# Kernel tuning notes

Hardware: AMD Instinct MI355X
Metric: run time of the kernel (lower is better)

Reference implementation:

```python
import jax, jax.numpy as jnp
import numpy as np

N, D, Z, T, K = 100000, 128, 128, 1024, 256
HID = 512
D_IN = D + 2 * Z  # concat of ctx, z_ctx_pe, z_tgt_pe


def setup_inputs() -> dict:
    key = jax.random.key(0)
    ks = jax.random.split(key, 12)
    inp = {
        'pe': jax.random.normal(ks[0], (N, 4), jnp.float32),
        'context_embedding': jax.random.normal(ks[1], (N, D), jnp.float32),
        'target_embedding': jax.random.normal(ks[2], (N, D), jnp.float32),
        # padded 2-hop subgraph node ids per target (precomputed k_hop_subgraph)
        'sub_nodes': jax.random.randint(ks[3], (T, K), 0, N, jnp.int32),
        'sub_counts': jax.random.randint(ks[4], (T,), 1, K + 1, jnp.int32),
        'target_nodes': jax.random.randint(ks[5], (T,), 0, N, jnp.int32),
        # params
        'z': jax.random.normal(ks[6], (1, Z), jnp.float32) * 0.1,
        'W_pe': jax.random.normal(ks[7], (4, Z), jnp.float32) * 0.5,
        'W1': jax.random.normal(ks[8], (D_IN, HID), jnp.float32) * (1.0 / np.sqrt(D_IN)),
        'b1': jnp.zeros((HID,), jnp.float32),
        'W2': jax.random.normal(ks[9], (HID, D), jnp.float32) * (1.0 / np.sqrt(HID)),
        'b2': jnp.zeros((D,), jnp.float32),
    }
    return inp


def reference(pe, context_embedding, target_embedding, sub_nodes, sub_counts,
              target_nodes, z, W_pe, W1, b1, W2, b2):
    # position_encoding = pe_projector(laplacian_eigenvector_pe)  [N, Z]
    pos_enc = pe @ W_pe
    # gather per-subgraph quantities (batched over T targets, padded to K)
    sub_ctx = context_embedding[sub_nodes]            # [T, K, D]
    z_ctx_pe = z + pos_enc[sub_nodes]                 # [T, K, Z]
    z_tgt_pe = z + pos_enc[target_nodes][:, None, :]  # [T, 1, Z] -> broadcast
    z_tgt_pe = jnp.broadcast_to(z_tgt_pe, z_ctx_pe.shape)
    agg = jnp.concatenate([sub_ctx, z_ctx_pe, z_tgt_pe], axis=-1)  # [T, K, D_IN]
    # predictor MLP
    pred = jax.nn.relu(agg @ W1 + b1) @ W2 + b2       # [T, K, D]
    tgt = target_embedding[target_nodes][:, None, :]  # [T, 1, D]
    sq = (pred - tgt) ** 2                            # [T, K, D]
    counts = jnp.maximum(sub_counts, 1)
    mask = (jnp.arange(K)[None, :] < counts[:, None]).astype(sq.dtype)  # [T, K]
    # per-target MSELoss (mean over n_sub * D elements), summed over targets
    per_target = jnp.sum(sq * mask[:, :, None], axis=(1, 2)) / (counts.astype(sq.dtype) * D)
    return jnp.sum(per_target)
```

## Files before the change

kernel.cpp:

```cpp
#include <hip/hip_runtime.h>
#include <hip/hip_bf16.h>

#define NN   100000
#define DD   128
#define ZZ   128
#define TT   1024
#define KK   256
#define HIDD 512

typedef __attribute__((ext_vector_type(8))) short  short8;
typedef __attribute__((ext_vector_type(4))) float  f32x4;

__device__ inline unsigned short f2bf(float f) {
    union { float f; unsigned int u; } x; x.f = f;
    unsigned int r = x.u + 0x7fffu + ((x.u >> 16) & 1u);
    return (unsigned short)(r >> 16);
}
__device__ inline void load_lds16(const void* g, void* l) {
    __builtin_amdgcn_global_load_lds((const __attribute__((address_space(1))) unsigned int*)g,
                                     (__attribute__((address_space(3))) unsigned int*)l, 16, 0, 0);
}

__global__ __launch_bounds__(256) void prep_tables(
    const float* __restrict__ pe, const float* __restrict__ ctx,
    const float* __restrict__ z, const float* __restrict__ wpe,
    unsigned short* __restrict__ ctx_bf, unsigned short* __restrict__ zpe_bf) {
    int g = blockIdx.x * 256 + threadIdx.x;
    if (g >= NN * 16) return;
    int n = g >> 4, j8 = (g & 15) << 3;
    float p0 = pe[n * 4 + 0], p1 = pe[n * 4 + 1], p2 = pe[n * 4 + 2], p3 = pe[n * 4 + 3];
    float4 c0 = *(const float4*)(ctx + (size_t)n * 128 + j8);
    float4 c1 = *(const float4*)(ctx + (size_t)n * 128 + j8 + 4);
    float4 z0 = *(const float4*)(z + j8);
    float4 z1 = *(const float4*)(z + j8 + 4);
    float4 wa0 = *(const float4*)(wpe + 0 * ZZ + j8), wa1 = *(const float4*)(wpe + 0 * ZZ + j8 + 4);
    float4 wb0 = *(const float4*)(wpe + 1 * ZZ + j8), wb1 = *(const float4*)(wpe + 1 * ZZ + j8 + 4);
    float4 wc0 = *(const float4*)(wpe + 2 * ZZ + j8), wc1 = *(const float4*)(wpe + 2 * ZZ + j8 + 4);
    float4 wd0 = *(const float4*)(wpe + 3 * ZZ + j8), wd1 = *(const float4*)(wpe + 3 * ZZ + j8 + 4);
    float zp[8], cv[8];
    zp[0] = z0.x + p0 * wa0.x + p1 * wb0.x + p2 * wc0.x + p3 * wd0.x;
    zp[1] = z0.y + p0 * wa0.y + p1 * wb0.y + p2 * wc0.y + p3 * wd0.y;
    zp[2] = z0.z + p0 * wa0.z + p1 * wb0.z + p2 * wc0.z + p3 * wd0.z;
    zp[3] = z0.w + p0 * wa0.w + p1 * wb0.w + p2 * wc0.w + p3 * wd0.w;
    zp[4] = z1.x + p0 * wa1.x + p1 * wb1.x + p2 * wc1.x + p3 * wd1.x;
    zp[5] = z1.y + p0 * wa1.y + p1 * wb1.y + p2 * wc1.y + p3 * wd1.y;
    zp[6] = z1.z + p0 * wa1.z + p1 * wb1.z + p2 * wc1.z + p3 * wd1.z;
    zp[7] = z1.w + p0 * wa1.w + p1 * wb1.w + p2 * wc1.w + p3 * wd1.w;
    cv[0] = c0.x; cv[1] = c0.y; cv[2] = c0.z; cv[3] = c0.w;
    cv[4] = c1.x; cv[5] = c1.y; cv[6] = c1.z; cv[7] = c1.w;
    short8 sz, sc;
#pragma unroll
    for (int i = 0; i < 8; ++i) { sz[i] = (short)f2bf(zp[i]); sc[i] = (short)f2bf(cv[i]); }
    *(short8*)(zpe_bf + (size_t)g * 8) = sz;
    *(short8*)(ctx_bf + (size_t)g * 8) = sc;
}

__global__ __launch_bounds__(256) void pack_ct(
    const float* __restrict__ W1, const float* __restrict__ W2,
    const float* __restrict__ pe, const float* __restrict__ z, const float* __restrict__ wpe,
    const int* __restrict__ target_nodes, const float* __restrict__ b1,
    unsigned short* __restrict__ w1p, unsigned short* __restrict__ w2p, float* __restrict__ ct_g) {
    __shared__ float zp[8][128];
    int tid = threadIdx.x;
    if (blockIdx.x < 768) {
        int g = blockIdx.x * 256 + tid;
        if (g < 256 * HIDD) {
            int e = g & 7, l = (g >> 3) & 63, tile = g >> 9;
            int ntg = tile & 7, rem = tile >> 3;
            int kc = rem & 7, hc = rem >> 3;
            int k = kc * 32 + (l >> 4) * 8 + e;
            int n = hc * 128 + ntg * 16 + (l & 15);
            w1p[g] = f2bf(W1[(size_t)k * HIDD + n]);
        } else {
            int q = g - 256 * HIDD;
            int e = q & 7, l = (q >> 3) & 63, tile = q >> 9;
            int ntg = tile & 7, kcg = tile >> 3;
            int k = kcg * 32 + (l >> 4) * 8 + e;
            int n = ntg * 16 + (l & 15);
            w2p[q] = f2bf(W2[(size_t)k * DD + n]);
        }
        return;
    }
    int b = blockIdx.x - 768;
#pragma unroll
    for (int q = 0; q < 4; ++q) {
        int idx = q * 256 + tid;
        int t8 = idx >> 7, zz = idx & 127;
        int tgt = target_nodes[b * 8 + t8];
        zp[t8][zz] = z[zz] + pe[tgt * 4 + 0] * wpe[zz] + pe[tgt * 4 + 1] * wpe[128 + zz]
                           + pe[tgt * 4 + 2] * wpe[256 + zz] + pe[tgt * 4 + 3] * wpe[384 + zz];
    }
    __syncthreads();
    int j0 = tid, j1 = tid + 256;
    float a0[8], a1[8];
    float bb0 = b1[j0], bb1 = b1[j1];
#pragma unroll
    for (int t8 = 0; t8 < 8; ++t8) { a0[t8] = bb0; a1[t8] = bb1; }
#pragma unroll 8
    for (int zz = 0; zz < 128; ++zz) {
        float w0 = W1[(size_t)(256 + zz) * HIDD + j0];
        float w1 = W1[(size_t)(256 + zz) * HIDD + j1];
#pragma unroll
        for (int t8 = 0; t8 < 8; ++t8) { a0[t8] += zp[t8][zz] * w0; a1[t8] += zp[t8][zz] * w1; }
    }
#pragma unroll
    for (int t8 = 0; t8 < 8; ++t8) {
        ct_g[(size_t)(b * 8 + t8) * HIDD + j0] = a0[t8];
        ct_g[(size_t)(b * 8 + t8) * HIDD + j1] = a1[t8];
    }
}

__global__ __launch_bounds__(256) void mp_jepa_main(
    const unsigned short* __restrict__ ctx_bf,
    const unsigned short* __restrict__ zpe_bf,
    const unsigned short* __restrict__ w1p,
    const unsigned short* __restrict__ w2p,
    const float* __restrict__ ct_g,
    const float* __restrict__ target_embedding,
    const int* __restrict__ sub_nodes,
    const int* __restrict__ sub_counts,
    const int* __restrict__ target_nodes,
    const float* __restrict__ b2,
    float* __restrict__ out) {
    const int bid = blockIdx.x;
    const int t = bid >> 2, kt = bid & 3;
    const int k0 = kt * 64;
    int cnt = sub_counts[t]; if (cnt < 1) cnt = 1;
    if (k0 >= cnt) return;
    const int tgt = target_nodes[t];

    __shared__ __align__(16) unsigned short ctxT[64 * 128];
    __shared__ __align__(16) unsigned short zpeT[64 * 128];
    __shared__ __align__(16) unsigned short hT[64 * 128];
    __shared__ float cts[HIDD];
    __shared__ float tgte[DD];
    __shared__ float b2s[DD];
    __shared__ float red[4];

    const int tid = threadIdx.x;
    const int w = tid >> 6, l = tid & 63;
    const int lo = l & 15, hi = l >> 4;

    {
        const char* cc = (const char*)ctx_bf;
        const char* zc = (const char*)zpe_bf;
        const int base = t * KK + k0;
#pragma unroll
        for (int it = 0; it < 4; ++it) {
            int rgrp = it * 16 + (w << 2);
            int row  = rgrp + hi;
            int node = sub_nodes[base + row];
            int soff = (lo << 4) ^ ((row & 7) << 4);
            load_lds16(cc + (size_t)node * 256 + soff, (char*)ctxT + rgrp * 256);
            load_lds16(zc + (size_t)node * 256 + soff, (char*)zpeT + rgrp * 256);
        }
    }
    if (tid < 128) {
        tgte[tid] = target_embedding[(size_t)tgt * 128 + tid];
        b2s[tid]  = b2[tid];
    }
    cts[tid]       = ct_g[(size_t)t * HIDD + tid];
    cts[tid + 256] = ct_g[(size_t)t * HIDD + tid + 256];
    __syncthreads();

    const short8* w1v = (const short8*)w1p;
    const short8* w2v = (const short8*)w2p;

    f32x4 accP[4][2];
#pragma unroll
    for (int rg = 0; rg < 4; ++rg)
#pragma unroll
        for (int nt = 0; nt < 2; ++nt) accP[rg][nt] = (f32x4){0.f, 0.f, 0.f, 0.f};

    for (int hc = 0; hc < 4; ++hc) {
        short8 wA[16];
#pragma unroll
        for (int i = 0; i < 16; ++i) {
            int kc = i >> 1, nt = i & 1;
            wA[i] = w1v[((((hc << 3) + kc) << 3) + (w << 1) + nt) * 64 + l];
        }
        f32x4 acc1[4][2];
#pragma unroll
        for (int nt = 0; nt < 2; ++nt) {
            f32x4 cv = *(const f32x4*)&cts[(hc << 7) + (((w << 1) + nt) << 4) + (hi << 2)];
#pragma unroll
            for (int rg = 0; rg < 4; ++rg) acc1[rg][nt] = cv;
        }
#pragma unroll
        for (int kc = 0; kc < 8; ++kc) {
            const unsigned short* src = (kc < 4) ? ctxT : zpeT;
            int cb = ((kc & 3) << 6) + (hi << 4);
            short8 a[4];
#pragma unroll
            for (int rg = 0; rg < 4; ++rg) {
                int row = (rg << 4) + lo;
                a[rg] = *(const short8*)(src + ((row * 256 + (cb ^ ((row & 7) << 4))) >> 1));
            }
#pragma unroll
            for (int rg = 0; rg < 4; ++rg) {
                acc1[rg][0] = __builtin_amdgcn_mfma_f32_16x16x32_bf16(wA[(kc << 1) + 0], a[rg], acc1[rg][0], 0, 0, 0);
                acc1[rg][1] = __builtin_amdgcn_mfma_f32_16x16x32_bf16(wA[(kc << 1) + 1], a[rg], acc1[rg][1], 0, 0, 0);
            }
        }

        short8 wB[8];
#pragma unroll
        for (int i = 0; i < 8; ++i) {
            int kc2 = i >> 1, nt = i & 1;
            wB[i] = w2v[((((hc << 2) + kc2) << 3) + (w << 1) + nt) * 64 + l];
        }

        __syncthreads();
#pragma unroll
        for (int nt = 0; nt < 2; ++nt) {
            int cbase = (((w << 1) + nt) << 5) + (hi << 3);
#pragma unroll
            for (int rg = 0; rg < 4; ++rg) {
                int row = (rg << 4) + lo;
                f32x4 v = acc1[rg][nt];
                float v0 = v[0] > 0.f ? v[0] : 0.f;
                float v1 = v[1] > 0.f ? v[1] : 0.f;
                float v2 = v[2] > 0.f ? v[2] : 0.f;
                float v3 = v[3] > 0.f ? v[3] : 0.f;
                uint2 p;
                p.x = (unsigned int)f2bf(v0) | ((unsigned int)f2bf(v1) << 16);
                p.y = (unsigned int)f2bf(v2) | ((unsigned int)f2bf(v3) << 16);
                *(uint2*)((char*)hT + row * 256 + (cbase ^ ((row & 7) << 4))) = p;
            }
        }
        __syncthreads();

#pragma unroll
        for (int kc2 = 0; kc2 < 4; ++kc2) {
            int cb = (kc2 << 6) + (hi << 4);
#pragma unroll
            for (int rg = 0; rg < 4; ++rg) {
                int row = (rg << 4) + lo;
                short8 a = *(const short8*)(hT + ((row * 256 + (cb ^ ((row & 7) << 4))) >> 1));
                accP[rg][0] = __builtin_amdgcn_mfma_f32_16x16x32_bf16(a, wB[(kc2 << 1) + 0], accP[rg][0], 0, 0, 0);
                accP[rg][1] = __builtin_amdgcn_mfma_f32_16x16x32_bf16(a, wB[(kc2 << 1) + 1], accP[rg][1], 0, 0, 0);
            }
        }
    }

    float s = 0.f;
#pragma unroll
    for (int nt = 0; nt < 2; ++nt) {
        int col = (w << 5) + (nt << 4) + lo;
        float bb = b2s[col] - tgte[col];
#pragma unroll
        for (int rg = 0; rg < 4; ++rg) {
#pragma unroll
            for (int r = 0; r < 4; ++r) {
                int row = (rg << 4) + (hi << 2) + r;
                float d = accP[rg][nt][r] + bb;
                if (k0 + row < cnt) s += d * d;
            }
        }
    }
#pragma unroll
    for (int off = 32; off > 0; off >>= 1) s += __shfl_xor(s, off, 64);
    if (l == 0) red[w] = s;
    __syncthreads();
    if (tid == 0) {
        float tot = (red[0] + red[1] + red[2] + red[3]) / ((float)cnt * 128.0f);
        atomicAdd(out, tot);
    }
}

extern "C" void kernel_launch(void* const* d_in, const int* in_sizes, int n_in,
                              void* d_out, int out_size, void* d_ws, size_t ws_size,
                              hipStream_t stream) {
    const float* pe           = (const float*)d_in[0];
    const float* ctx          = (const float*)d_in[1];
    const float* tgt_emb      = (const float*)d_in[2];
    const int*   sub_nodes    = (const int*)d_in[3];
    const int*   sub_counts   = (const int*)d_in[4];
    const int*   target_nodes = (const int*)d_in[5];
    const float* z            = (const float*)d_in[6];
    const float* wpe          = (const float*)d_in[7];
    const float* W1           = (const float*)d_in[8];
    const float* b1           = (const float*)d_in[9];
    const float* W2           = (const float*)d_in[10];
    const float* b2           = (const float*)d_in[11];
    float* out = (float*)d_out;

    char* ws = (char*)d_ws;
    unsigned short* ctx_bf = (unsigned short*)ws;
    unsigned short* zpe_bf = (unsigned short*)(ws + 25600000);
    unsigned short* w1p    = (unsigned short*)(ws + 51200000);
    unsigned short* w2p    = (unsigned short*)(ws + 51200000 + 262144);
    float*          ct_g   = (float*)(ws + 51200000 + 262144 + 131072);

    hipMemsetAsync(d_out, 0, sizeof(float), stream);
    prep_tables<<<(NN * 16 + 255) / 256, 256, 0, stream>>>(pe, ctx, z, wpe, ctx_bf, zpe_bf);
    pack_ct<<<896, 256, 0, stream>>>(W1, W2, pe, z, wpe, target_nodes, b1, w1p, w2p, ct_g);
    mp_jepa_main<<<TT * 4, 256, 0, stream>>>(ctx_bf, zpe_bf, w1p, w2p, ct_g, tgt_emb,
                                             sub_nodes, sub_counts, target_nodes, b2, out);
}
```

Before: 280.3 us.

## Keep hidden activations in registers and split second GEMM over K with LDS reduction

The W1 packing is permuted so each wave's first-GEMM accumulator layout matches the A-operand layout of the second GEMM. ReLU'd hidden values then feed the W2 MFMAs straight from registers, which removes the hT LDS round trip and two barriers per hidden chunk. Each wave now produces partial sums for all 128 output columns over its own K slice. The four partials are reduced through swizzled LDS buffers at the end. This costs more accumulator registers (32 f32x4 per wave), a larger LDS footprint with a final cross-wave reduction, and launch bounds now requesting 2 blocks per SM.

New measurement: 467.1 us. 1.67x slower.

```diff
diff --git a/kernel.cpp b/kernel.cpp
--- a/kernel.cpp
+++ b/kernel.cpp
@@ -69,7 +69,8 @@
             int ntg = tile & 7, rem = tile >> 3;
             int kc = rem & 7, hc = rem >> 3;
             int k = kc * 32 + (l >> 4) * 8 + e;
-            int n = hc * 128 + ntg * 16 + (l & 15);
+            int o = l & 15;
+            int n = hc * 128 + (ntg >> 1) * 32 + ((o >> 2) << 3) + (o & 3) + ((ntg & 1) << 2);
             w1p[g] = f2bf(W1[(size_t)k * HIDD + n]);
         } else {
             int q = g - 256 * HIDD;
@@ -110,7 +111,7 @@
     }
 }
 
-__global__ __launch_bounds__(256) void mp_jepa_main(
+__global__ __launch_bounds__(256, 2) void mp_jepa_main(
     const unsigned short* __restrict__ ctx_bf,
     const unsigned short* __restrict__ zpe_bf,
     const unsigned short* __restrict__ w1p,
@@ -129,13 +130,15 @@
     if (k0 >= cnt) return;
     const int tgt = target_nodes[t];
 
-    __shared__ __align__(16) unsigned short ctxT[64 * 128];
-    __shared__ __align__(16) unsigned short zpeT[64 * 128];
-    __shared__ __align__(16) unsigned short hT[64 * 128];
-    __shared__ float cts[HIDD];
+    __shared__ __align__(16) char smem[32768];
+    __shared__ __align__(16) float psumB[8192];
+    __shared__ __align__(16) float cts[HIDD];
     __shared__ float tgte[DD];
     __shared__ float b2s[DD];
     __shared__ float red[4];
+    unsigned short* ctxT = (unsigned short*)smem;
+    unsigned short* zpeT = (unsigned short*)(smem + 16384);
+    float* psumA = (float*)smem;
 
     const int tid = threadIdx.x;
     const int w = tid >> 6, l = tid & 63;
@@ -166,28 +169,25 @@
     const short8* w1v = (const short8*)w1p;
     const short8* w2v = (const short8*)w2p;
 
-    f32x4 accP[4][2];
+    f32x4 accP[4][8];
 #pragma unroll
     for (int rg = 0; rg < 4; ++rg)
 #pragma unroll
-        for (int nt = 0; nt < 2; ++nt) accP[rg][nt] = (f32x4){0.f, 0.f, 0.f, 0.f};
-
+        for (int nt8 = 0; nt8 < 8; ++nt8) accP[rg][nt8] = (f32x4){0.f, 0.f, 0.f, 0.f};
+
+#pragma unroll
     for (int hc = 0; hc < 4; ++hc) {
-        short8 wA[16];
-#pragma unroll
-        for (int i = 0; i < 16; ++i) {
-            int kc = i >> 1, nt = i & 1;
-            wA[i] = w1v[((((hc << 3) + kc) << 3) + (w << 1) + nt) * 64 + l];
-        }
         f32x4 acc1[4][2];
 #pragma unroll
         for (int nt = 0; nt < 2; ++nt) {
-            f32x4 cv = *(const f32x4*)&cts[(hc << 7) + (((w << 1) + nt) << 4) + (hi << 2)];
+            f32x4 cv = *(const f32x4*)&cts[(hc << 7) + (w << 5) + (hi << 3) + (nt << 2)];
 #pragma unroll
             for (int rg = 0; rg < 4; ++rg) acc1[rg][nt] = cv;
         }
 #pragma unroll
         for (int kc = 0; kc < 8; ++kc) {
+            short8 bf0 = w1v[((((hc << 3) + kc) << 3) + (w << 1) + 0) * 64 + l];
+            short8 bf1 = w1v[((((hc << 3) + kc) << 3) + (w << 1) + 1) * 64 + l];
             const unsigned short* src = (kc < 4) ? ctxT : zpeT;
             int cb = ((kc & 3) << 6) + (hi << 4);
             short8 a[4];
@@ -198,64 +198,67 @@
             }
 #pragma unroll
             for (int rg = 0; rg < 4; ++rg) {
-                acc1[rg][0] = __builtin_amdgcn_mfma_f32_16x16x32_bf16(wA[(kc << 1) + 0], a[rg], acc1[rg][0], 0, 0, 0);
-                acc1[rg][1] = __builtin_amdgcn_mfma_f32_16x16x32_bf16(wA[(kc << 1) + 1], a[rg], acc1[rg][1], 0, 0, 0);
+                acc1[rg][0] = __builtin_amdgcn_mfma_f32_16x16x32_bf16(bf0, a[rg], acc1[rg][0], 0, 0, 0);
+                acc1[rg][1] = __builtin_amdgcn_mfma_f32_16x16x32_bf16(bf1, a[rg], acc1[rg][1], 0, 0, 0);
             }
         }
-
-        short8 wB[8];
-#pragma unroll
-        for (int i = 0; i < 8; ++i) {
-            int kc2 = i >> 1, nt = i & 1;
-            wB[i] = w2v[((((hc << 2) + kc2) << 3) + (w << 1) + nt) * 64 + l];
-        }
-
-        __syncthreads();
-#pragma unroll
-        for (int nt = 0; nt < 2; ++nt) {
-            int cbase = (((w << 1) + nt) << 5) + (hi << 3);
-#pragma unroll
-            for (int rg = 0; rg < 4; ++rg) {
-                int row = (rg << 4) + lo;
-                f32x4 v = acc1[rg][nt];
-                float v0 = v[0] > 0.f ? v[0] : 0.f;
-                float v1 = v[1] > 0.f ? v[1] : 0.f;
-                float v2 = v[2] > 0.f ? v[2] : 0.f;
-                float v3 = v[3] > 0.f ? v[3] : 0.f;
-                uint2 p;
-                p.x = (unsigned int)f2bf(v0) | ((unsigned int)f2bf(v1) << 16);
-                p.y = (unsigned int)f2bf(v2) | ((unsigned int)f2bf(v3) << 16);
-                *(uint2*)((char*)hT + row * 256 + (cbase ^ ((row & 7) << 4))) = p;
+        short8 a32[4];
+#pragma unroll
+        for (int rg = 0; rg < 4; ++rg) {
+#pragma unroll
+            for (int e = 0; e < 4; ++e) {
+                float v0 = acc1[rg][0][e]; v0 = v0 > 0.f ? v0 : 0.f;
+                float v1 = acc1[rg][1][e]; v1 = v1 > 0.f ? v1 : 0.f;
+                a32[rg][e]     = (short)f2bf(v0);
+                a32[rg][e + 4] = (short)f2bf(v1);
             }
         }
-        __syncthreads();
-
-#pragma unroll
-        for (int kc2 = 0; kc2 < 4; ++kc2) {
-            int cb = (kc2 << 6) + (hi << 4);
-#pragma unroll
-            for (int rg = 0; rg < 4; ++rg) {
-                int row = (rg << 4) + lo;
-                short8 a = *(const short8*)(hT + ((row * 256 + (cb ^ ((row & 7) << 4))) >> 1));
-                accP[rg][0] = __builtin_amdgcn_mfma_f32_16x16x32_bf16(a, wB[(kc2 << 1) + 0], accP[rg][0], 0, 0, 0);
-                accP[rg][1] = __builtin_amdgcn_mfma_f32_16x16x32_bf16(a, wB[(kc2 << 1) + 1], accP[rg][1], 0, 0, 0);
-            }
-        }
-    }
+        int kcg = (hc << 2) + w;
+#pragma unroll
+        for (int nt8 = 0; nt8 < 8; ++nt8) {
+            short8 wb = w2v[((kcg << 3) + nt8) * 64 + l];
+#pragma unroll
+            for (int rg = 0; rg < 4; ++rg)
+                accP[rg][nt8] = __builtin_amdgcn_mfma_f32_16x16x32_bf16(a32[rg], wb, accP[rg][nt8], 0, 0, 0);
+        }
+    }
+
+    __syncthreads();
+#pragma unroll
+    for (int rg = 0; rg < 4; ++rg)
+#pragma unroll
+        for (int nt8 = 0; nt8 < 8; ++nt8) {
+            int col = (nt8 << 4) + lo;
+            int word = ((col << 6) + (rg << 4) + (hi << 2)) ^ ((col & 7) << 2);
+            if (w == 0) *(f32x4*)(psumA + word) = accP[rg][nt8];
+            if (w == 1) *(f32x4*)(psumB + word) = accP[rg][nt8];
+        }
+    __syncthreads();
+#pragma unroll
+    for (int rg = 0; rg < 4; ++rg)
+#pragma unroll
+        for (int nt8 = 0; nt8 < 8; ++nt8) {
+            int col = (nt8 << 4) + lo;
+            int word = ((col << 6) + (rg << 4) + (hi << 2)) ^ ((col & 7) << 2);
+            if (w == 2) { f32x4 v = *(f32x4*)(psumA + word); v += accP[rg][nt8]; *(f32x4*)(psumA + word) = v; }
+            if (w == 3) { f32x4 v = *(f32x4*)(psumB + word); v += accP[rg][nt8]; *(f32x4*)(psumB + word) = v; }
+        }
+    __syncthreads();
 
     float s = 0.f;
 #pragma unroll
-    for (int nt = 0; nt < 2; ++nt) {
-        int col = (w << 5) + (nt << 4) + lo;
+    for (int rq = 0; rq < 8; ++rq) {
+        int base = (rq << 10) + (tid << 2);
+        int col = base >> 6;
+        int row0 = base & 63;
+        int word = base ^ ((col & 7) << 2);
+        f32x4 va = *(const f32x4*)(psumA + word);
+        f32x4 vb = *(const f32x4*)(psumB + word);
         float bb = b2s[col] - tgte[col];
 #pragma unroll
-        for (int rg = 0; rg < 4; ++rg) {
-#pragma unroll
-            for (int r = 0; r < 4; ++r) {
-                int row = (rg << 4) + (hi << 2) + r;
-                float d = accP[rg][nt][r] + bb;
-                if (k0 + row < cnt) s += d * d;
-            }
+        for (int r = 0; r < 4; ++r) {
+            float d = va[r] + vb[r] + bb;
+            if (k0 + row0 + r < cnt) s += d * d;
         }
     }
 #pragma unroll
```

## Split main kernel work over 8 waves in a 2x4 grid, stream weights per k-step

Applied to the files above, without the earlier changes.

Raises the main kernel's block to 512 threads and arranges the 8 waves as 2 row halves by 4 column groups, so each wave holds half the rows' accumulators. W1/W2 fragments are now loaded per k-step instead of being preloaded into 16+8 registers, which cuts register pressure. Block indexing is reordered so the k-tile index is the slow dimension, grouping blocks by tile position and putting the mostly-empty later tiles at the end. The cost is that each W1/W2 fragment is now fetched by twice as many waves, and the per-step loads add latency that the MFMAs must hide.

Result: faster. 248.9 us (-11.2%).

```diff
diff --git a/kernel.cpp b/kernel.cpp
--- a/kernel.cpp
+++ b/kernel.cpp
@@ -110,7 +110,7 @@
     }
 }
 
-__global__ __launch_bounds__(256) void mp_jepa_main(
+__global__ __launch_bounds__(512) void mp_jepa_main(
     const unsigned short* __restrict__ ctx_bf,
     const unsigned short* __restrict__ zpe_bf,
     const unsigned short* __restrict__ w1p,
@@ -123,7 +123,7 @@
     const float* __restrict__ b2,
     float* __restrict__ out) {
     const int bid = blockIdx.x;
-    const int t = bid >> 2, kt = bid & 3;
+    const int kt = bid >> 10, t = bid & 1023;
     const int k0 = kt * 64;
     int cnt = sub_counts[t]; if (cnt < 1) cnt = 1;
     if (k0 >= cnt) return;
@@ -135,10 +135,11 @@
     __shared__ float cts[HIDD];
     __shared__ float tgte[DD];
     __shared__ float b2s[DD];
-    __shared__ float red[4];
+    __shared__ float red[8];
 
     const int tid = threadIdx.x;
     const int w = tid >> 6, l = tid & 63;
+    const int wm = w & 1, wn = w >> 1;
     const int lo = l & 15, hi = l >> 4;
 
     {
@@ -146,8 +147,8 @@
         const char* zc = (const char*)zpe_bf;
         const int base = t * KK + k0;
 #pragma unroll
-        for (int it = 0; it < 4; ++it) {
-            int rgrp = it * 16 + (w << 2);
+        for (int it = 0; it < 2; ++it) {
+            int rgrp = it * 32 + (w << 2);
             int row  = rgrp + hi;
             int node = sub_nodes[base + row];
             int soff = (lo << 4) ^ ((row & 7) << 4);
@@ -159,64 +160,52 @@
         tgte[tid] = target_embedding[(size_t)tgt * 128 + tid];
         b2s[tid]  = b2[tid];
     }
-    cts[tid]       = ct_g[(size_t)t * HIDD + tid];
-    cts[tid + 256] = ct_g[(size_t)t * HIDD + tid + 256];
+    cts[tid] = ct_g[(size_t)t * HIDD + tid];
     __syncthreads();
 
     const short8* w1v = (const short8*)w1p;
     const short8* w2v = (const short8*)w2p;
 
-    f32x4 accP[4][2];
-#pragma unroll
-    for (int rg = 0; rg < 4; ++rg)
+    f32x4 accP[2][2];
+#pragma unroll
+    for (int rg = 0; rg < 2; ++rg)
 #pragma unroll
         for (int nt = 0; nt < 2; ++nt) accP[rg][nt] = (f32x4){0.f, 0.f, 0.f, 0.f};
 
     for (int hc = 0; hc < 4; ++hc) {
-        short8 wA[16];
-#pragma unroll
-        for (int i = 0; i < 16; ++i) {
-            int kc = i >> 1, nt = i & 1;
-            wA[i] = w1v[((((hc << 3) + kc) << 3) + (w << 1) + nt) * 64 + l];
-        }
-        f32x4 acc1[4][2];
+        f32x4 acc1[2][2];
 #pragma unroll
         for (int nt = 0; nt < 2; ++nt) {
-            f32x4 cv = *(const f32x4*)&cts[(hc << 7) + (((w << 1) + nt) << 4) + (hi << 2)];
-#pragma unroll
-            for (int rg = 0; rg < 4; ++rg) acc1[rg][nt] = cv;
+            f32x4 cv = *(const f32x4*)&cts[(hc << 7) + (((wn << 1) + nt) << 4) + (hi << 2)];
+            acc1[0][nt] = cv;
+            acc1[1][nt] = cv;
         }
 #pragma unroll
         for (int kc = 0; kc < 8; ++kc) {
+            short8 bf0 = w1v[((((hc << 3) + kc) << 3) + (wn << 1) + 0) * 64 + l];
+            short8 bf1 = w1v[((((hc << 3) + kc) << 3) + (wn << 1) + 1) * 64 + l];
             const unsigned short* src = (kc < 4) ? ctxT : zpeT;
             int cb = ((kc & 3) << 6) + (hi << 4);
-            short8 a[4];
-#pragma unroll
-            for (int rg = 0; rg < 4; ++rg) {
-                int row = (rg << 4) + lo;
+            short8 a[2];
+#pragma unroll
+            for (int rg = 0; rg < 2; ++rg) {
+                int row = (wm << 5) + (rg << 4) + lo;
                 a[rg] = *(const short8*)(src + ((row * 256 + (cb ^ ((row & 7) << 4))) >> 1));
             }
 #pragma unroll
-            for (int rg = 0; rg < 4; ++rg) {
-                acc1[rg][0] = __builtin_amdgcn_mfma_f32_16x16x32_bf16(wA[(kc << 1) + 0], a[rg], acc1[rg][0], 0, 0, 0);
-                acc1[rg][1] = __builtin_amdgcn_mfma_f32_16x16x32_bf16(wA[(kc << 1) + 1], a[rg], acc1[rg][1], 0, 0, 0);
-            }
-        }
-
-        short8 wB[8];
-#pragma unroll
-        for (int i = 0; i < 8; ++i) {
-            int kc2 = i >> 1, nt = i & 1;
-            wB[i] = w2v[((((hc << 2) + kc2) << 3) + (w << 1) + nt) * 64 + l];
+            for (int rg = 0; rg < 2; ++rg) {
+                acc1[rg][0] = __builtin_amdgcn_mfma_f32_16x16x32_bf16(bf0, a[rg], acc1[rg][0], 0, 0, 0);
+                acc1[rg][1] = __builtin_amdgcn_mfma_f32_16x16x32_bf16(bf1, a[rg], acc1[rg][1], 0, 0, 0);
+            }
         }
 
         __syncthreads();
 #pragma unroll
         for (int nt = 0; nt < 2; ++nt) {
-            int cbase = (((w << 1) + nt) << 5) + (hi << 3);
-#pragma unroll
-            for (int rg = 0; rg < 4; ++rg) {
-                int row = (rg << 4) + lo;
+            int cbase = (((wn << 1) + nt) << 5) + (hi << 3);
+#pragma unroll
+            for (int rg = 0; rg < 2; ++rg) {
+                int row = (wm << 5) + (rg << 4) + lo;
                 f32x4 v = acc1[rg][nt];
                 float v0 = v[0] > 0.f ? v[0] : 0.f;
                 float v1 = v[1] > 0.f ? v[1] : 0.f;
@@ -232,13 +221,15 @@
 
 #pragma unroll
         for (int kc2 = 0; kc2 < 4; ++kc2) {
+            short8 bg0 = w2v[((((hc << 2) + kc2) << 3) + (wn << 1) + 0) * 64 + l];
+            short8 bg1 = w2v[((((hc << 2) + kc2) << 3) + (wn << 1) + 1) * 64 + l];
             int cb = (kc2 << 6) + (hi << 4);
 #pragma unroll
-            for (int rg = 0; rg < 4; ++rg) {
-                int row = (rg << 4) + lo;
+            for (int rg = 0; rg < 2; ++rg) {
+                int row = (wm << 5) + (rg << 4) + lo;
                 short8 a = *(const short8*)(hT + ((row * 256 + (cb ^ ((row & 7) << 4))) >> 1));
-                accP[rg][0] = __builtin_amdgcn_mfma_f32_16x16x32_bf16(a, wB[(kc2 << 1) + 0], accP[rg][0], 0, 0, 0);
-                accP[rg][1] = __builtin_amdgcn_mfma_f32_16x16x32_bf16(a, wB[(kc2 << 1) + 1], accP[rg][1], 0, 0, 0);
+                accP[rg][0] = __builtin_amdgcn_mfma_f32_16x16x32_bf16(a, bg0, accP[rg][0], 0, 0, 0);
+                accP[rg][1] = __builtin_amdgcn_mfma_f32_16x16x32_bf16(a, bg1, accP[rg][1], 0, 0, 0);
             }
         }
     }
@@ -246,13 +237,13 @@
     float s = 0.f;
 #pragma unroll
     for (int nt = 0; nt < 2; ++nt) {
-        int col = (w << 5) + (nt << 4) + lo;
+        int col = (((wn << 1) + nt) << 4) + lo;
         float bb = b2s[col] - tgte[col];
 #pragma unroll
-        for (int rg = 0; rg < 4; ++rg) {
+        for (int rg = 0; rg < 2; ++rg) {
 #pragma unroll
             for (int r = 0; r < 4; ++r) {
-                int row = (rg << 4) + (hi << 2) + r;
+                int row = (wm << 5) + (rg << 4) + (hi << 2) + r;
                 float d = accP[rg][nt][r] + bb;
                 if (k0 + row < cnt) s += d * d;
             }
@@ -263,7 +254,8 @@
     if (l == 0) red[w] = s;
     __syncthreads();
     if (tid == 0) {
-        float tot = (red[0] + red[1] + red[2] + red[3]) / ((float)cnt * 128.0f);
+        float tot = (red[0] + red[1] + red[2] + red[3] + red[4] + red[5] + red[6] + red[7])
+                    / ((float)cnt * 128.0f);
         atomicAdd(out, tot);
     }
 }
@@ -295,6 +287,6 @@
     hipMemsetAsync(d_out, 0, sizeof(float), stream);
     prep_tables<<<(NN * 16 + 255) / 256, 256, 0, stream>>>(pe, ctx, z, wpe, ctx_bf, zpe_bf);
     pack_ct<<<896, 256, 0, stream>>>(W1, W2, pe, z, wpe, target_nodes, b1, w1p, w2p, ct_g);
-    mp_jepa_main<<<TT * 4, 256, 0, stream>>>(ctx_bf, zpe_bf, w1p, w2p, ct_g, tgt_emb,
+    mp_jepa_main<<<TT * 4, 512, 0, stream>>>(ctx_bf, zpe_bf, w1p, w2p, ct_g, tgt_emb,
                                              sub_nodes, sub_counts, target_nodes, b2, out);
 }
```
